# Kernel tuning notes

Hardware: AMD Instinct MI355X
Metric: run time of the kernel (lower is better)

Reference implementation:

```python
import jax, jax.numpy as jnp
import numpy as np


def setup_inputs() -> dict:
    key = jax.random.key(0)
    k1, k2, k3 = jax.random.split(key, 3)
    shape = (16, 128, 128, 64)  # [B, H, W, C]
    return {
        "query": jax.random.normal(k1, shape, dtype=jnp.float32),
        "keys": jax.random.normal(k2, shape, dtype=jnp.float32),
        "values": jax.random.normal(k3, shape, dtype=jnp.float32),
    }


def reference(query, keys, values):
    # Attention over channel dim C, feature dim = H*W.
    # scores[b, q, k] = sum_{h,w} Q[b,h,w,q] * K[b,h,w,k]
    scores = jnp.einsum("bhwq,bhwk->bqk", query, keys)
    attn = jax.nn.softmax(scores, axis=-1)  # softmax over keys k
    # out[b,h,w,q] = sum_k attn[b,q,k] * V[b,h,w,k]
    out = jnp.einsum("bqk,bhwk->bhwq", attn, values)
    return out
```

## Files before the change

### kernel.cpp

```cpp
#include <hip/hip_runtime.h>


#define S_SPLIT 32
#define CHUNK (16384 / S_SPLIT)
#define TILE_ROWS 32
#define NT (CHUNK / TILE_ROWS)

__global__ __launch_bounds__(256) void scores_kernel(
    const float* __restrict__ Q, const float* __restrict__ K,
    float* __restrict__ partial) {
  const int bs = blockIdx.x;
  const int b = bs / S_SPLIT;
  const int s = bs % S_SPLIT;
  const int tid = threadIdx.x;
  const int w = tid >> 6;
  const int l = tid & 63;
  const int q0 = (l >> 3) * 8;
  const int k0 = (l & 7) * 8;

  __shared__ union {
    struct { float4 q[2][512]; float4 k[2][512]; } t;
    float red[2][4096];
  } lds;

  float acc[8][8];
#pragma unroll
  for (int i = 0; i < 8; ++i)
#pragma unroll
    for (int j = 0; j < 8; ++j) acc[i][j] = 0.f;

  const float4* Qg = (const float4*)(Q + ((size_t)b * 16384 + (size_t)s * CHUNK) * 64);
  const float4* Kg = (const float4*)(K + ((size_t)b * 16384 + (size_t)s * CHUNK) * 64);

  lds.t.q[0][tid]       = Qg[tid];
  lds.t.q[0][tid + 256] = Qg[tid + 256];
  lds.t.k[0][tid]       = Kg[tid];
  lds.t.k[0][tid + 256] = Kg[tid + 256];

  for (int t = 0; t < NT; ++t) {
    __syncthreads();
    const int cb = t & 1;

    float4 pq0, pq1, pk0, pk1;
    if (t + 1 < NT) {
      pq0 = Qg[(t + 1) * 512 + tid];
      pq1 = Qg[(t + 1) * 512 + tid + 256];
      pk0 = Kg[(t + 1) * 512 + tid];
      pk1 = Kg[(t + 1) * 512 + tid + 256];
    }

#pragma unroll
    for (int i = 0; i < 8; ++i) {
      const int r = (i << 2) + w;
      float4 qa = lds.t.q[cb][r * 16 + (q0 >> 2)];
      float4 qb = lds.t.q[cb][r * 16 + (q0 >> 2) + 1];
      float4 ka = lds.t.k[cb][r * 16 + (k0 >> 2)];
      float4 kb = lds.t.k[cb][r * 16 + (k0 >> 2) + 1];
      float qv[8] = {qa.x, qa.y, qa.z, qa.w, qb.x, qb.y, qb.z, qb.w};
      float kv[8] = {ka.x, ka.y, ka.z, ka.w, kb.x, kb.y, kb.z, kb.w};
#pragma unroll
      for (int ii = 0; ii < 8; ++ii)
#pragma unroll
        for (int jj = 0; jj < 8; ++jj)
          acc[ii][jj] += qv[ii] * kv[jj];
    }

    if (t + 1 < NT) {
      const int nb = (t + 1) & 1;
      lds.t.q[nb][tid]       = pq0;
      lds.t.q[nb][tid + 256] = pq1;
      lds.t.k[nb][tid]       = pk0;
      lds.t.k[nb][tid + 256] = pk1;
    }
  }

  __syncthreads();
  if (w >= 2) {
    float4* dst = (float4*)lds.red[w - 2];
#pragma unroll
    for (int i = 0; i < 8; ++i) {
      dst[(q0 + i) * 16 + (k0 >> 2)]     = make_float4(acc[i][0], acc[i][1], acc[i][2], acc[i][3]);
      dst[(q0 + i) * 16 + (k0 >> 2) + 1] = make_float4(acc[i][4], acc[i][5], acc[i][6], acc[i][7]);
    }
  }
  __syncthreads();
  if (w < 2) {
    float4* dst = (float4*)lds.red[w];
#pragma unroll
    for (int i = 0; i < 8; ++i) {
      float4 u = dst[(q0 + i) * 16 + (k0 >> 2)];
      float4 v = dst[(q0 + i) * 16 + (k0 >> 2) + 1];
      dst[(q0 + i) * 16 + (k0 >> 2)]     = make_float4(u.x + acc[i][0], u.y + acc[i][1], u.z + acc[i][2], u.w + acc[i][3]);
      dst[(q0 + i) * 16 + (k0 >> 2) + 1] = make_float4(v.x + acc[i][4], v.y + acc[i][5], v.z + acc[i][6], v.w + acc[i][7]);
    }
  }
  __syncthreads();
  float4* p4 = (float4*)(partial + (size_t)bs * 4096);
  const float4* r0 = (const float4*)lds.red[0];
  const float4* r1 = (const float4*)lds.red[1];
#pragma unroll
  for (int c = 0; c < 4; ++c) {
    float4 x = r0[c * 256 + tid];
    float4 y = r1[c * 256 + tid];
    p4[c * 256 + tid] = make_float4(x.x + y.x, x.y + y.y, x.z + y.z, x.w + y.w);
  }
}

__global__ __launch_bounds__(64) void softmax_kernel(
    const float* __restrict__ partial, float* __restrict__ attn_t) {
  const int blk = blockIdx.x;
  const int b = blk >> 4;
  const int q0 = (blk & 15) * 4;
  const int lane = threadIdx.x;
  const int ql = lane >> 4;
  const int k4 = lane & 15;

  const float4* P = (const float4*)partial;
  float4 v = make_float4(0.f, 0.f, 0.f, 0.f);
  for (int s = 0; s < S_SPLIT; ++s) {
    float4 t = P[((size_t)(b * S_SPLIT + s) * 64 + q0 + ql) * 16 + k4];
    v.x += t.x; v.y += t.y; v.z += t.z; v.w += t.w;
  }

  float m = fmaxf(fmaxf(v.x, v.y), fmaxf(v.z, v.w));
#pragma unroll
  for (int off = 8; off > 0; off >>= 1)
    m = fmaxf(m, __shfl_xor(m, off, 64));
  float4 e = make_float4(__expf(v.x - m), __expf(v.y - m), __expf(v.z - m), __expf(v.w - m));
  float sum = e.x + e.y + e.z + e.w;
#pragma unroll
  for (int off = 8; off > 0; off >>= 1)
    sum += __shfl_xor(sum, off, 64);
  const float inv = 1.f / sum;

  float* A = attn_t + (size_t)b * 4096;
  A[(4 * k4 + 0) * 64 + q0 + ql] = e.x * inv;
  A[(4 * k4 + 1) * 64 + q0 + ql] = e.y * inv;
  A[(4 * k4 + 2) * 64 + q0 + ql] = e.z * inv;
  A[(4 * k4 + 3) * 64 + q0 + ql] = e.w * inv;
}

__global__ __launch_bounds__(256) void out_kernel(
    const float* __restrict__ V, const float* __restrict__ attn_t,
    float* __restrict__ out) {
  const int blk = blockIdx.x;
  const int b = blk >> 7;
  const int tile = blk & 127;
  const int tid = threadIdx.x;
  const int g = tid >> 4;
  const int qg = tid & 15;

  __shared__ float4 Vl[128 * 17];
  __shared__ float4 Al[64 * 16];

  const float4* Vg = (const float4*)(V + ((size_t)b * 16384 + (size_t)tile * 128) * 64);
#pragma unroll
  for (int u = 0; u < 8; ++u) {
    const int idx = u * 256 + tid;
    Vl[(idx >> 4) * 17 + (idx & 15)] = Vg[idx];
  }
  const float4* Ag = (const float4*)(attn_t + (size_t)b * 4096);
#pragma unroll
  for (int u = 0; u < 4; ++u)
    Al[u * 256 + tid] = Ag[u * 256 + tid];
  __syncthreads();

  float acc[8][4];
#pragma unroll
  for (int i = 0; i < 8; ++i)
#pragma unroll
    for (int j = 0; j < 4; ++j) acc[i][j] = 0.f;

  for (int k4 = 0; k4 < 16; ++k4) {
    const float4 a0 = Al[(4 * k4 + 0) * 16 + qg];
    const float4 a1 = Al[(4 * k4 + 1) * 16 + qg];
    const float4 a2 = Al[(4 * k4 + 2) * 16 + qg];
    const float4 a3 = Al[(4 * k4 + 3) * 16 + qg];
#pragma unroll
    for (int i = 0; i < 8; ++i) {
      const float4 v = Vl[(i * 16 + g) * 17 + k4];
      acc[i][0] += v.x * a0.x + v.y * a1.x + v.z * a2.x + v.w * a3.x;
      acc[i][1] += v.x * a0.y + v.y * a1.y + v.z * a2.y + v.w * a3.y;
      acc[i][2] += v.x * a0.z + v.y * a1.z + v.z * a2.z + v.w * a3.z;
      acc[i][3] += v.x * a0.w + v.y * a1.w + v.z * a2.w + v.w * a3.w;
    }
  }

  float4* og = (float4*)(out + ((size_t)b * 16384 + (size_t)tile * 128) * 64);
#pragma unroll
  for (int i = 0; i < 8; ++i) {
    const int row = i * 16 + g;
    og[row * 16 + qg] = make_float4(acc[i][0], acc[i][1], acc[i][2], acc[i][3]);
  }
}

extern "C" void kernel_launch(void* const* d_in, const int* in_sizes, int n_in,
                              void* d_out, int out_size, void* d_ws, size_t ws_size,
                              hipStream_t stream) {
  const float* Q = (const float*)d_in[0];
  const float* K = (const float*)d_in[1];
  const float* V = (const float*)d_in[2];
  float* out = (float*)d_out;

  float* partial = (float*)d_ws;
  float* attn_t = partial + (size_t)16 * S_SPLIT * 4096;

  scores_kernel<<<16 * S_SPLIT, 256, 0, stream>>>(Q, K, partial);
  softmax_kernel<<<16 * 16, 64, 0, stream>>>(partial, attn_t);
  out_kernel<<<16 * 128, 256, 0, stream>>>(V, attn_t, out);
}
```

Before: 227.3 us.

## Raise scores split to 64 and make output kernel one row per thread

The scores kernel is templated on the split count, and the launcher uses 64 splits when the workspace is large enough, doubling block count for better occupancy on the reduction. The output kernel now has each thread own one spatial row and compute all 64 output channels in registers. It reads the attention matrix straight from global memory (uniform across the wave, so it can be scalar loads) instead of staging V and attention in LDS. This removes LDS traffic and syncs but uses many registers and makes V loads per-thread strided (each thread reads its own 256-byte row).

```diff
diff --git a/kernel.cpp b/kernel.cpp
--- a/kernel.cpp
+++ b/kernel.cpp
@@ -1,17 +1,17 @@
 #include <hip/hip_runtime.h>
 
 
-#define S_SPLIT 32
-#define CHUNK (16384 / S_SPLIT)
 #define TILE_ROWS 32
-#define NT (CHUNK / TILE_ROWS)
-
+
+template <int SPLIT>
 __global__ __launch_bounds__(256) void scores_kernel(
     const float* __restrict__ Q, const float* __restrict__ K,
     float* __restrict__ partial) {
+  constexpr int CH = 16384 / SPLIT;
+  constexpr int NT = CH / TILE_ROWS;
   const int bs = blockIdx.x;
-  const int b = bs / S_SPLIT;
-  const int s = bs % S_SPLIT;
+  const int b = bs / SPLIT;
+  const int s = bs % SPLIT;
   const int tid = threadIdx.x;
   const int w = tid >> 6;
   const int l = tid & 63;
@@ -29,8 +29,8 @@
 #pragma unroll
     for (int j = 0; j < 8; ++j) acc[i][j] = 0.f;
 
-  const float4* Qg = (const float4*)(Q + ((size_t)b * 16384 + (size_t)s * CHUNK) * 64);
-  const float4* Kg = (const float4*)(K + ((size_t)b * 16384 + (size_t)s * CHUNK) * 64);
+  const float4* Qg = (const float4*)(Q + ((size_t)b * 16384 + (size_t)s * CH) * 64);
+  const float4* Kg = (const float4*)(K + ((size_t)b * 16384 + (size_t)s * CH) * 64);
 
   lds.t.q[0][tid]       = Qg[tid];
   lds.t.q[0][tid + 256] = Qg[tid + 256];
@@ -106,6 +106,7 @@
   }
 }
 
+template <int SPLIT>
 __global__ __launch_bounds__(64) void softmax_kernel(
     const float* __restrict__ partial, float* __restrict__ attn_t) {
   const int blk = blockIdx.x;
@@ -117,8 +118,8 @@
 
   const float4* P = (const float4*)partial;
   float4 v = make_float4(0.f, 0.f, 0.f, 0.f);
-  for (int s = 0; s < S_SPLIT; ++s) {
-    float4 t = P[((size_t)(b * S_SPLIT + s) * 64 + q0 + ql) * 16 + k4];
+  for (int s = 0; s < SPLIT; ++s) {
+    float4 t = P[((size_t)(b * SPLIT + s) * 64 + q0 + ql) * 16 + k4];
     v.x += t.x; v.y += t.y; v.z += t.z; v.w += t.w;
   }
 
@@ -140,58 +141,37 @@
   A[(4 * k4 + 3) * 64 + q0 + ql] = e.w * inv;
 }
 
-__global__ __launch_bounds__(256) void out_kernel(
+__global__ __launch_bounds__(64) void out_kernel(
     const float* __restrict__ V, const float* __restrict__ attn_t,
     float* __restrict__ out) {
   const int blk = blockIdx.x;
-  const int b = blk >> 7;
-  const int tile = blk & 127;
-  const int tid = threadIdx.x;
-  const int g = tid >> 4;
-  const int qg = tid & 15;
-
-  __shared__ float4 Vl[128 * 17];
-  __shared__ float4 Al[64 * 16];
-
-  const float4* Vg = (const float4*)(V + ((size_t)b * 16384 + (size_t)tile * 128) * 64);
-#pragma unroll
-  for (int u = 0; u < 8; ++u) {
-    const int idx = u * 256 + tid;
-    Vl[(idx >> 4) * 17 + (idx & 15)] = Vg[idx];
-  }
-  const float4* Ag = (const float4*)(attn_t + (size_t)b * 4096);
-#pragma unroll
-  for (int u = 0; u < 4; ++u)
-    Al[u * 256 + tid] = Ag[u * 256 + tid];
-  __syncthreads();
-
-  float acc[8][4];
-#pragma unroll
-  for (int i = 0; i < 8; ++i)
-#pragma unroll
-    for (int j = 0; j < 4; ++j) acc[i][j] = 0.f;
-
+  const int b = blk >> 8;
+  const int tile = blk & 255;
+  const int row = tile * 64 + (int)threadIdx.x;
+
+  const float4* V4 = (const float4*)(V + ((size_t)b * 16384 + row) * 64);
+  const float* A = attn_t + (size_t)b * 4096;
+
+  float acc[64];
+#pragma unroll
+  for (int q = 0; q < 64; ++q) acc[q] = 0.f;
+
+  float4 vv = V4[0];
   for (int k4 = 0; k4 < 16; ++k4) {
-    const float4 a0 = Al[(4 * k4 + 0) * 16 + qg];
-    const float4 a1 = Al[(4 * k4 + 1) * 16 + qg];
-    const float4 a2 = Al[(4 * k4 + 2) * 16 + qg];
-    const float4 a3 = Al[(4 * k4 + 3) * 16 + qg];
-#pragma unroll
-    for (int i = 0; i < 8; ++i) {
-      const float4 v = Vl[(i * 16 + g) * 17 + k4];
-      acc[i][0] += v.x * a0.x + v.y * a1.x + v.z * a2.x + v.w * a3.x;
-      acc[i][1] += v.x * a0.y + v.y * a1.y + v.z * a2.y + v.w * a3.y;
-      acc[i][2] += v.x * a0.z + v.y * a1.z + v.z * a2.z + v.w * a3.z;
-      acc[i][3] += v.x * a0.w + v.y * a1.w + v.z * a2.w + v.w * a3.w;
-    }
-  }
-
-  float4* og = (float4*)(out + ((size_t)b * 16384 + (size_t)tile * 128) * 64);
-#pragma unroll
-  for (int i = 0; i < 8; ++i) {
-    const int row = i * 16 + g;
-    og[row * 16 + qg] = make_float4(acc[i][0], acc[i][1], acc[i][2], acc[i][3]);
-  }
+    float4 vn = vv;
+    if (k4 < 15) vn = V4[k4 + 1];
+    const float* A0 = A + (size_t)(4 * k4) * 64;
+#pragma unroll
+    for (int q = 0; q < 64; ++q) {
+      acc[q] += vv.x * A0[q] + vv.y * A0[64 + q] + vv.z * A0[128 + q] + vv.w * A0[192 + q];
+    }
+    vv = vn;
+  }
+
+  float4* og = (float4*)(out + ((size_t)b * 16384 + row) * 64);
+#pragma unroll
+  for (int q4 = 0; q4 < 16; ++q4)
+    og[q4] = make_float4(acc[4 * q4], acc[4 * q4 + 1], acc[4 * q4 + 2], acc[4 * q4 + 3]);
 }
 
 extern "C" void kernel_launch(void* const* d_in, const int* in_sizes, int n_in,
@@ -202,10 +182,19 @@
   const float* V = (const float*)d_in[2];
   float* out = (float*)d_out;
 
-  float* partial = (float*)d_ws;
-  float* attn_t = partial + (size_t)16 * S_SPLIT * 4096;
-
-  scores_kernel<<<16 * S_SPLIT, 256, 0, stream>>>(Q, K, partial);
-  softmax_kernel<<<16 * 16, 64, 0, stream>>>(partial, attn_t);
-  out_kernel<<<16 * 128, 256, 0, stream>>>(V, attn_t, out);
-}
+  const size_t need64 = (size_t)16 * 64 * 4096 * 4 + (size_t)16 * 4096 * 4;
+
+  if (ws_size >= need64) {
+    float* partial = (float*)d_ws;
+    float* attn_t = partial + (size_t)16 * 64 * 4096;
+    scores_kernel<64><<<16 * 64, 256, 0, stream>>>(Q, K, partial);
+    softmax_kernel<64><<<16 * 16, 64, 0, stream>>>(partial, attn_t);
+    out_kernel<<<16 * 256, 64, 0, stream>>>(V, attn_t, out);
+  } else {
+    float* partial = (float*)d_ws;
+    float* attn_t = partial + (size_t)16 * 32 * 4096;
+    scores_kernel<32><<<16 * 32, 256, 0, stream>>>(Q, K, partial);
+    softmax_kernel<32><<<16 * 16, 64, 0, stream>>>(partial, attn_t);
+    out_kernel<<<16 * 256, 64, 0, stream>>>(V, attn_t, out);
+  }
+}
```

New measurement: 253.8 us. 11.7% more time.

## Fuse three kernels into one cooperative kernel with grid-wide syncs

Applied to the files above, without the earlier changes.

Merges the scores, softmax and output kernels into a single cooperative launch of 512 blocks that separates the phases with grid.sync(), falling back to the three separate launches if the cooperative launch fails. Each block computes its score partial, then 64 blocks run the softmax tasks, then each block loads attention into shared memory once and produces four output tiles. This is meant to remove kernel launch gaps and repeated attention loads. In exchange the output phase drops from 2048 blocks to 512, and during softmax most blocks sit idle at the barrier.

```diff
diff --git a/kernel.cpp b/kernel.cpp
--- a/kernel.cpp
+++ b/kernel.cpp
@@ -1,36 +1,36 @@
 #include <hip/hip_runtime.h>
-
-
-#define S_SPLIT 32
-#define CHUNK (16384 / S_SPLIT)
-#define TILE_ROWS 32
-#define NT (CHUNK / TILE_ROWS)
-
-__global__ __launch_bounds__(256) void scores_kernel(
+#include <hip/hip_cooperative_groups.h>
+
+namespace cg = cooperative_groups;
+
+
+#define SPLITN 32
+#define NT 16
+
+union LdsU {
+  struct { float4 q[2][512]; float4 k[2][512]; } t;
+  float red[2][4096];
+  struct { float4 v[128 * 17]; float4 a[64 * 16]; } c;
+};
+
+__device__ __forceinline__ void scores_phase(LdsU& lds,
     const float* __restrict__ Q, const float* __restrict__ K,
-    float* __restrict__ partial) {
-  const int bs = blockIdx.x;
-  const int b = bs / S_SPLIT;
-  const int s = bs % S_SPLIT;
-  const int tid = threadIdx.x;
+    float* __restrict__ partial, int bs, int tid) {
+  const int b = bs >> 5;
+  const int s = bs & 31;
   const int w = tid >> 6;
   const int l = tid & 63;
   const int q0 = (l >> 3) * 8;
   const int k0 = (l & 7) * 8;
 
-  __shared__ union {
-    struct { float4 q[2][512]; float4 k[2][512]; } t;
-    float red[2][4096];
-  } lds;
-
   float acc[8][8];
 #pragma unroll
   for (int i = 0; i < 8; ++i)
 #pragma unroll
     for (int j = 0; j < 8; ++j) acc[i][j] = 0.f;
 
-  const float4* Qg = (const float4*)(Q + ((size_t)b * 16384 + (size_t)s * CHUNK) * 64);
-  const float4* Kg = (const float4*)(K + ((size_t)b * 16384 + (size_t)s * CHUNK) * 64);
+  const float4* Qg = (const float4*)(Q + ((size_t)b * 16384 + (size_t)s * 512) * 64);
+  const float4* Kg = (const float4*)(K + ((size_t)b * 16384 + (size_t)s * 512) * 64);
 
   lds.t.q[0][tid]       = Qg[tid];
   lds.t.q[0][tid + 256] = Qg[tid + 256];
@@ -106,19 +106,17 @@
   }
 }
 
-__global__ __launch_bounds__(64) void softmax_kernel(
-    const float* __restrict__ partial, float* __restrict__ attn_t) {
-  const int blk = blockIdx.x;
-  const int b = blk >> 4;
-  const int q0 = (blk & 15) * 4;
-  const int lane = threadIdx.x;
-  const int ql = lane >> 4;
-  const int k4 = lane & 15;
+__device__ __forceinline__ void softmax_task(
+    const float* __restrict__ partial, float* __restrict__ attn_t, int task, int l) {
+  const int b = task >> 4;
+  const int q0 = (task & 15) * 4;
+  const int ql = l >> 4;
+  const int k4 = l & 15;
 
   const float4* P = (const float4*)partial;
   float4 v = make_float4(0.f, 0.f, 0.f, 0.f);
-  for (int s = 0; s < S_SPLIT; ++s) {
-    float4 t = P[((size_t)(b * S_SPLIT + s) * 64 + q0 + ql) * 16 + k4];
+  for (int s = 0; s < SPLITN; ++s) {
+    float4 t = P[((size_t)(b * SPLITN + s) * 64 + q0 + ql) * 16 + k4];
     v.x += t.x; v.y += t.y; v.z += t.z; v.w += t.w;
   }
 
@@ -140,29 +138,25 @@
   A[(4 * k4 + 3) * 64 + q0 + ql] = e.w * inv;
 }
 
-__global__ __launch_bounds__(256) void out_kernel(
-    const float* __restrict__ V, const float* __restrict__ attn_t,
-    float* __restrict__ out) {
-  const int blk = blockIdx.x;
-  const int b = blk >> 7;
-  const int tile = blk & 127;
-  const int tid = threadIdx.x;
+__device__ __forceinline__ void load_attn_lds(LdsU& lds, const float* __restrict__ attn_t,
+                                              int b, int tid) {
+  const float4* Ag = (const float4*)(attn_t + (size_t)b * 4096);
+#pragma unroll
+  for (int u = 0; u < 4; ++u)
+    lds.c.a[u * 256 + tid] = Ag[u * 256 + tid];
+}
+
+__device__ __forceinline__ void out_tile(LdsU& lds, const float* __restrict__ V,
+                                         float* __restrict__ out, int b, int tile, int tid) {
   const int g = tid >> 4;
   const int qg = tid & 15;
 
-  __shared__ float4 Vl[128 * 17];
-  __shared__ float4 Al[64 * 16];
-
   const float4* Vg = (const float4*)(V + ((size_t)b * 16384 + (size_t)tile * 128) * 64);
 #pragma unroll
   for (int u = 0; u < 8; ++u) {
     const int idx = u * 256 + tid;
-    Vl[(idx >> 4) * 17 + (idx & 15)] = Vg[idx];
-  }
-  const float4* Ag = (const float4*)(attn_t + (size_t)b * 4096);
-#pragma unroll
-  for (int u = 0; u < 4; ++u)
-    Al[u * 256 + tid] = Ag[u * 256 + tid];
+    lds.c.v[(idx >> 4) * 17 + (idx & 15)] = Vg[idx];
+  }
   __syncthreads();
 
   float acc[8][4];
@@ -172,13 +166,13 @@
     for (int j = 0; j < 4; ++j) acc[i][j] = 0.f;
 
   for (int k4 = 0; k4 < 16; ++k4) {
-    const float4 a0 = Al[(4 * k4 + 0) * 16 + qg];
-    const float4 a1 = Al[(4 * k4 + 1) * 16 + qg];
-    const float4 a2 = Al[(4 * k4 + 2) * 16 + qg];
-    const float4 a3 = Al[(4 * k4 + 3) * 16 + qg];
-#pragma unroll
-    for (int i = 0; i < 8; ++i) {
-      const float4 v = Vl[(i * 16 + g) * 17 + k4];
+    const float4 a0 = lds.c.a[(4 * k4 + 0) * 16 + qg];
+    const float4 a1 = lds.c.a[(4 * k4 + 1) * 16 + qg];
+    const float4 a2 = lds.c.a[(4 * k4 + 2) * 16 + qg];
+    const float4 a3 = lds.c.a[(4 * k4 + 3) * 16 + qg];
+#pragma unroll
+    for (int i = 0; i < 8; ++i) {
+      const float4 v = lds.c.v[(i * 16 + g) * 17 + k4];
       acc[i][0] += v.x * a0.x + v.y * a1.x + v.z * a2.x + v.w * a3.x;
       acc[i][1] += v.x * a0.y + v.y * a1.y + v.z * a2.y + v.w * a3.y;
       acc[i][2] += v.x * a0.z + v.y * a1.z + v.z * a2.z + v.w * a3.z;
@@ -192,6 +186,58 @@
     const int row = i * 16 + g;
     og[row * 16 + qg] = make_float4(acc[i][0], acc[i][1], acc[i][2], acc[i][3]);
   }
+}
+
+__global__ __launch_bounds__(256, 3) void fused_kernel(
+    const float* __restrict__ Q, const float* __restrict__ K,
+    const float* __restrict__ V, float* __restrict__ out,
+    float* __restrict__ partial, float* __restrict__ attn_t) {
+  const int blk = blockIdx.x;
+  const int tid = threadIdx.x;
+  const int w = tid >> 6;
+  const int l = tid & 63;
+
+  __shared__ LdsU lds;
+
+  cg::grid_group grid = cg::this_grid();
+
+  scores_phase(lds, Q, K, partial, blk, tid);
+
+  grid.sync();
+
+  if (blk < 64) softmax_task(partial, attn_t, (blk << 2) + w, l);
+
+  grid.sync();
+
+  {
+    const int b = blk >> 5;
+    load_attn_lds(lds, attn_t, b, tid);
+    for (int it = 0; it < 4; ++it) {
+      if (it) __syncthreads();
+      out_tile(lds, V, out, b, ((blk & 31) << 2) + it, tid);
+    }
+  }
+}
+
+__global__ __launch_bounds__(256) void scores_kernel(
+    const float* __restrict__ Q, const float* __restrict__ K,
+    float* __restrict__ partial) {
+  __shared__ LdsU lds;
+  scores_phase(lds, Q, K, partial, blockIdx.x, threadIdx.x);
+}
+
+__global__ __launch_bounds__(64) void softmax_kernel(
+    const float* __restrict__ partial, float* __restrict__ attn_t) {
+  softmax_task(partial, attn_t, blockIdx.x, threadIdx.x);
+}
+
+__global__ __launch_bounds__(256) void out_kernel(
+    const float* __restrict__ V, const float* __restrict__ attn_t,
+    float* __restrict__ out) {
+  __shared__ LdsU lds;
+  const int b = blockIdx.x >> 7;
+  load_attn_lds(lds, attn_t, b, threadIdx.x);
+  out_tile(lds, V, out, b, blockIdx.x & 127, threadIdx.x);
 }
 
 extern "C" void kernel_launch(void* const* d_in, const int* in_sizes, int n_in,
@@ -203,9 +249,15 @@
   float* out = (float*)d_out;
 
   float* partial = (float*)d_ws;
-  float* attn_t = partial + (size_t)16 * S_SPLIT * 4096;
-
-  scores_kernel<<<16 * S_SPLIT, 256, 0, stream>>>(Q, K, partial);
-  softmax_kernel<<<16 * 16, 64, 0, stream>>>(partial, attn_t);
-  out_kernel<<<16 * 128, 256, 0, stream>>>(V, attn_t, out);
-}
+  float* attn_t = partial + (size_t)16 * SPLITN * 4096;
+
+  void* args[] = {(void*)&Q, (void*)&K, (void*)&V, (void*)&out,
+                  (void*)&partial, (void*)&attn_t};
+  hipError_t err = hipLaunchCooperativeKernel((const void*)fused_kernel,
+                                              dim3(512), dim3(256), args, 0, stream);
+  if (err != hipSuccess) {
+    scores_kernel<<<16 * SPLITN, 256, 0, stream>>>(Q, K, partial);
+    softmax_kernel<<<16 * 16  * 1, 64, 0, stream>>>(partial, attn_t);
+    out_kernel<<<16 * 128, 256, 0, stream>>>(V, attn_t, out);
+  }
+}
```

Result: slower. 380.6 us (+67.5%).
